# Kernel optimization log

Measured on AMD Instinct MI355X. Metric: run time of the kernel, lower is better.

Reference implementation:

```python
import jax, jax.numpy as jnp
from jax import lax
import numpy as np

B, S, D, H = 256, 4096, 64, 128  # batch, seq_len, input_dim, hidden_dim


def setup_inputs() -> dict:
    key = jax.random.key(0)
    ks = jax.random.split(key, 6)
    s_i = 1.0 / np.sqrt(D)
    s_h = 1.0 / np.sqrt(H)
    return {
        "x": jax.random.normal(ks[0], (B, S, D), dtype=jnp.float32),
        "Wi": jax.random.uniform(ks[1], (D, 4 * H), jnp.float32, -s_i, s_i),  # input->gates, no bias (flax LSTMCell)
        "Wh": jax.random.uniform(ks[2], (H, 4 * H), jnp.float32, -s_h, s_h),  # hidden->gates
        "bh": jnp.zeros((4 * H,), jnp.float32),
        "Wo": jax.random.uniform(ks[3], (H, 1), jnp.float32, -s_h, s_h),      # output Dense
        "bo": jnp.zeros((1,), jnp.float32),
    }


def reference(x, Wi, Wh, bh, Wo, bo):
    b, s, _ = x.shape
    h_dim = Wh.shape[0]
    # Precompute the input-path gate projections for all timesteps at once.
    xg = jnp.einsum('bsd,dg->sbg', x, Wi)  # [S, B, 4H]

    def step(carry, xg_t):
        c, h = carry
        z = xg_t + h @ Wh + bh  # [B, 4H]
        i, f, g, o = jnp.split(z, 4, axis=-1)
        i = jax.nn.sigmoid(i)
        f = jax.nn.sigmoid(f)
        g = jnp.tanh(g)
        o = jax.nn.sigmoid(o)
        c_new = f * c + i * g
        h_new = o * jnp.tanh(c_new)
        return (c_new, h_new), None

    c0 = jnp.zeros((b, h_dim), x.dtype)
    h0 = jnp.zeros((b, h_dim), x.dtype)
    (c_last, h_last), _ = lax.scan(step, (c0, h0), xg)
    # project last hidden state -> (batch, 1)
    return h_last @ Wo + bo
```

## Files before the change

### kernel.cpp

```cpp
#include <hip/hip_runtime.h>
#include <hip/hip_fp16.h>


#define LSTM_B 256
#define LSTM_S 4096
#define LSTM_D 64
#define LSTM_H 128
#define LSTM_G 512

typedef _Float16 f16x8 __attribute__((ext_vector_type(8)));
typedef float f32x4 __attribute__((ext_vector_type(4)));

__device__ __forceinline__ float sigm(float z) {
  return __builtin_amdgcn_rcpf(1.0f + __builtin_amdgcn_exp2f(-1.44269504f * z));
}
__device__ __forceinline__ float tanh_(float z) {
  return 1.0f - 2.0f * __builtin_amdgcn_rcpf(1.0f + __builtin_amdgcn_exp2f(2.88539008f * z));
}

__global__ __launch_bounds__(256, 1)
void lstm_mfma_kernel(const float* __restrict__ x,
                      const float* __restrict__ Wi,
                      const float* __restrict__ Wh,
                      const float* __restrict__ bh,
                      const float* __restrict__ Wo,
                      const float* __restrict__ bo,
                      float* __restrict__ out) {
  const int t    = threadIdx.x;
  const int lane = t & 63;
  const int w    = t >> 6;
  const int b    = blockIdx.x;
  const int lmod = lane & 15;
  const int lgrp = lane >> 4;

  __shared__ __align__(16) _Float16 Hbuf[2][LSTM_H];
  __shared__ __align__(16) _Float16 Xbuf[2][LSTM_D];
  __shared__ __align__(16) _Float16 Zr[8];
  __shared__ float R[LSTM_H];

  f16x8 Bf[8][6];
  #pragma unroll
  for (int g = 0; g < 4; ++g) {
    #pragma unroll
    for (int hh = 0; hh < 2; ++hh) {
      const int nt = 2 * g + hh;
      const int n = 128 * g + 32 * w + 16 * hh + lmod;
      #pragma unroll
      for (int kk = 0; kk < 6; ++kk) {
        union { f16x8 v; _Float16 e[8]; } uB;
        #pragma unroll
        for (int j = 0; j < 8; ++j) {
          const int k = 32 * kk + 8 * lgrp + j;
          const float val = (k < LSTM_H) ? Wh[(size_t)k * LSTM_G + n]
                                         : Wi[(size_t)(k - LSTM_H) * LSTM_G + n];
          uB.e[j] = (_Float16)val;
        }
        Bf[nt][kk] = uB.v;
      }
    }
  }

  const int ul = 32 * w + (lane & 31);
  const float bb0 = bh[ul];
  const float bb1 = bh[LSTM_H + ul];
  const float bb2 = bh[2 * LSTM_H + ul];
  const float bb3 = bh[3 * LSTM_H + ul];

  const float* xb = x + (size_t)b * (LSTM_S * LSTM_D);
  const bool areal = (lmod == 0) || (lmod == 4);

  const f32x4 ZQ = {0.f, 0.f, 0.f, 0.f};

  if (t < LSTM_H) Hbuf[0][t] = (_Float16)0.0f;
  if (w == 1) Xbuf[0][lane] = (_Float16)xb[lane];
  if (w == 2) Xbuf[1][lane] = (_Float16)xb[LSTM_D + lane];
  if (t < 8) Zr[t] = (_Float16)0.0f;
  __syncthreads();

  f16x8 X0a, X0b, X1a, X1b;
  f32x4 accP[8], accQ[8];
  {
    const char* a0 = areal ? ((const char*)&Xbuf[0][0] + 16 * lgrp)
                           : (const char*)&Zr[0];
    const int s0 = areal ? 64 : 0;
    f16x8 T0 = *(const f16x8*)(a0);
    f16x8 T1 = *(const f16x8*)(a0 + s0);
    const char* a1 = areal ? ((const char*)&Xbuf[1][0] + 16 * lgrp)
                           : (const char*)&Zr[0];
    X0a = *(const f16x8*)(a1);
    X0b = *(const f16x8*)(a1 + s0);
    #pragma unroll
    for (int n = 0; n < 8; ++n) {
      accP[n] = __builtin_amdgcn_mfma_f32_16x16x32_f16(T0, Bf[n][4], ZQ, 0, 0, 0);
      accP[n] = __builtin_amdgcn_mfma_f32_16x16x32_f16(T1, Bf[n][5], accP[n], 0, 0, 0);
    }
  }
  __syncthreads();
  if (w == 1) Xbuf[0][lane] = (_Float16)xb[2 * LSTM_D + lane];
  float xA = 0.f, xB = 0.f;
  if (w == 3) {
    xA = xb[3 * LSTM_D + lane];
    xB = xb[4 * LSTM_D + lane];
  }
  float c = 0.f, hval = 0.f;
  __syncthreads();

  #define STEPB(P, ACCIN, ACCOUT, XC0, XC1, XN0, XN1)                          \
  {                                                                            \
    float xn = 0.f;                                                            \
    if (w == 3) {                                                              \
      int si = s + 5; if (si > LSTM_S - 1) si = LSTM_S - 1;                    \
      xn = xb[(size_t)si * LSTM_D + lane];                                     \
    }                                                                          \
    const char* ahB = areal ? ((const char*)&Hbuf[P][0] + 16 * lgrp)           \
                            : (const char*)&Zr[0];                             \
    const int ahS = areal ? 64 : 0;                                            \
    f16x8 Ah0 = *(const f16x8*)(ahB);                                          \
    f16x8 Ah1 = *(const f16x8*)(ahB + 1 * ahS);                                \
    f16x8 Ah2 = *(const f16x8*)(ahB + 2 * ahS);                                \
    f16x8 Ah3 = *(const f16x8*)(ahB + 3 * ahS);                                \
    const char* axB = areal ? ((const char*)&Xbuf[P][0] + 16 * lgrp)           \
                            : (const char*)&Zr[0];                             \
    XN0 = *(const f16x8*)(axB);                                                \
    XN1 = *(const f16x8*)(axB + ahS);                                          \
    __builtin_amdgcn_sched_barrier(0);                                         \
    _Pragma("unroll")                                                          \
    for (int n = 0; n < 8; ++n)                                                \
      ACCOUT[n] = __builtin_amdgcn_mfma_f32_16x16x32_f16(XC0, Bf[n][4], ZQ, 0, 0, 0); \
    _Pragma("unroll")                                                          \
    for (int n = 0; n < 8; ++n)                                                \
      ACCOUT[n] = __builtin_amdgcn_mfma_f32_16x16x32_f16(XC1, Bf[n][5], ACCOUT[n], 0, 0, 0); \
    __builtin_amdgcn_sched_barrier(0);                                         \
    _Pragma("unroll")                                                          \
    for (int n = 0; n < 8; ++n)                                                \
      ACCIN[n] = __builtin_amdgcn_mfma_f32_16x16x32_f16(Ah0, Bf[n][0], ACCIN[n], 0, 0, 0); \
    _Pragma("unroll")                                                          \
    for (int n = 0; n < 8; ++n)                                                \
      ACCIN[n] = __builtin_amdgcn_mfma_f32_16x16x32_f16(Ah1, Bf[n][1], ACCIN[n], 0, 0, 0); \
    _Pragma("unroll")                                                          \
    for (int n = 0; n < 8; ++n)                                                \
      ACCIN[n] = __builtin_amdgcn_mfma_f32_16x16x32_f16(Ah2, Bf[n][2], ACCIN[n], 0, 0, 0); \
    _Pragma("unroll")                                                          \
    for (int n = 0; n < 8; ++n)                                                \
      ACCIN[n] = __builtin_amdgcn_mfma_f32_16x16x32_f16(Ah3, Bf[n][3], ACCIN[n], 0, 0, 0); \
    {                                                                          \
      const bool hsel = (lane & 16) != 0;                                      \
      const float zi = (hsel ? ACCIN[1][0] : ACCIN[0][0]) + bb0;               \
      const float zf = (hsel ? ACCIN[3][0] : ACCIN[2][0]) + bb1;               \
      const float zg = (hsel ? ACCIN[5][0] : ACCIN[4][0]) + bb2;               \
      const float zo = (hsel ? ACCIN[7][0] : ACCIN[6][0]) + bb3;               \
      const float iv = sigm(zi);                                               \
      const float fv = sigm(zf);                                               \
      const float gv = tanh_(zg);                                              \
      const float ov = sigm(zo);                                               \
      c = fv * c + iv * gv;                                                    \
      hval = ov * tanh_(c);                                                    \
      if (lane < 32) Hbuf[(P) ^ 1][ul] = (_Float16)hval;                       \
    }                                                                          \
    if (w == 3) {                                                              \
      Xbuf[(P) ^ 1][lane] = (_Float16)xA;                                      \
      xA = xB;                                                                 \
      xB = xn;                                                                 \
    }                                                                          \
    __syncthreads();                                                           \
  }

  for (int s = 0; s < LSTM_S; s += 2) {
    STEPB(0, accP, accQ, X0a, X0b, X1a, X1b)
    ++s;
    STEPB(1, accQ, accP, X1a, X1b, X0a, X0b)
    --s;
  }
  #undef STEPB

  if (lane < 32) R[ul] = hval * Wo[ul];
  __syncthreads();
  if (t < 64) {
    float v = R[t] + R[t + 64];
    #pragma unroll
    for (int off = 32; off; off >>= 1) v += __shfl_down(v, off);
    if (t == 0) out[b] = v + bo[0];
  }
}

extern "C" void kernel_launch(void* const* d_in, const int* in_sizes, int n_in,
                              void* d_out, int out_size, void* d_ws, size_t ws_size,
                              hipStream_t stream) {
  const float* x  = (const float*)d_in[0];
  const float* Wi = (const float*)d_in[1];
  const float* Wh = (const float*)d_in[2];
  const float* bh = (const float*)d_in[3];
  const float* Wo = (const float*)d_in[4];
  const float* bo = (const float*)d_in[5];
  float* out = (float*)d_out;

  lstm_mfma_kernel<<<LSTM_B, 256, 0, stream>>>(x, Wi, Wh, bh, Wo, bo, out);
}
```

Baseline: 2.216 ms.

## Split LSTM gate columns across eight waves instead of four per block

Each block now runs 512 threads (8 waves). Each wave owns 16 hidden units and computes 4 MFMA N-tiles per step instead of 8, which halves the per-wave serial MFMA chain on the recurrent critical path. The cost is more waves synchronising at every timestep barrier. The 8 waves also share the SIMDs, so MFMA throughput per CU may not improve, and only 16 lanes per wave now do the gate math.

```diff
diff --git a/kernel.cpp b/kernel.cpp
--- a/kernel.cpp
+++ b/kernel.cpp
@@ -11,6 +11,8 @@
 typedef _Float16 f16x8 __attribute__((ext_vector_type(8)));
 typedef float f32x4 __attribute__((ext_vector_type(4)));
 
+#define SBAR() __builtin_amdgcn_sched_barrier(0)
+
 __device__ __forceinline__ float sigm(float z) {
   return __builtin_amdgcn_rcpf(1.0f + __builtin_amdgcn_exp2f(-1.44269504f * z));
 }
@@ -18,7 +20,7 @@
   return 1.0f - 2.0f * __builtin_amdgcn_rcpf(1.0f + __builtin_amdgcn_exp2f(2.88539008f * z));
 }
 
-__global__ __launch_bounds__(256, 1)
+__global__ __launch_bounds__(512, 2)
 void lstm_mfma_kernel(const float* __restrict__ x,
                       const float* __restrict__ Wi,
                       const float* __restrict__ Wh,
@@ -38,36 +40,32 @@
   __shared__ __align__(16) _Float16 Zr[8];
   __shared__ float R[LSTM_H];
 
-  f16x8 Bf[8][6];
+  f16x8 Bf[4][6];
   #pragma unroll
   for (int g = 0; g < 4; ++g) {
+    const int n = 128 * g + 16 * w + lmod;
     #pragma unroll
-    for (int hh = 0; hh < 2; ++hh) {
-      const int nt = 2 * g + hh;
-      const int n = 128 * g + 32 * w + 16 * hh + lmod;
+    for (int kk = 0; kk < 6; ++kk) {
+      union { f16x8 v; _Float16 e[8]; } uB;
       #pragma unroll
-      for (int kk = 0; kk < 6; ++kk) {
-        union { f16x8 v; _Float16 e[8]; } uB;
-        #pragma unroll
-        for (int j = 0; j < 8; ++j) {
-          const int k = 32 * kk + 8 * lgrp + j;
-          const float val = (k < LSTM_H) ? Wh[(size_t)k * LSTM_G + n]
-                                         : Wi[(size_t)(k - LSTM_H) * LSTM_G + n];
-          uB.e[j] = (_Float16)val;
-        }
-        Bf[nt][kk] = uB.v;
+      for (int j = 0; j < 8; ++j) {
+        const int k = 32 * kk + 8 * lgrp + j;
+        const float val = (k < LSTM_H) ? Wh[(size_t)k * LSTM_G + n]
+                                       : Wi[(size_t)(k - LSTM_H) * LSTM_G + n];
+        uB.e[j] = (_Float16)val;
       }
+      Bf[g][kk] = uB.v;
     }
   }
 
-  const int ul = 32 * w + (lane & 31);
+  const int ul = 16 * w + lmod;
   const float bb0 = bh[ul];
   const float bb1 = bh[LSTM_H + ul];
   const float bb2 = bh[2 * LSTM_H + ul];
   const float bb3 = bh[3 * LSTM_H + ul];
 
   const float* xb = x + (size_t)b * (LSTM_S * LSTM_D);
-  const bool areal = (lmod == 0) || (lmod == 4);
+  const bool areal = (lmod == 0);
 
   const f32x4 ZQ = {0.f, 0.f, 0.f, 0.f};
 
@@ -78,7 +76,7 @@
   __syncthreads();
 
   f16x8 X0a, X0b, X1a, X1b;
-  f32x4 accP[8], accQ[8];
+  f32x4 accP[4], accQ[4];
   {
     const char* a0 = areal ? ((const char*)&Xbuf[0][0] + 16 * lgrp)
                            : (const char*)&Zr[0];
@@ -90,25 +88,27 @@
     X0a = *(const f16x8*)(a1);
     X0b = *(const f16x8*)(a1 + s0);
     #pragma unroll
-    for (int n = 0; n < 8; ++n) {
-      accP[n] = __builtin_amdgcn_mfma_f32_16x16x32_f16(T0, Bf[n][4], ZQ, 0, 0, 0);
-      accP[n] = __builtin_amdgcn_mfma_f32_16x16x32_f16(T1, Bf[n][5], accP[n], 0, 0, 0);
+    for (int g = 0; g < 4; ++g) {
+      accP[g] = __builtin_amdgcn_mfma_f32_16x16x32_f16(T0, Bf[g][4], ZQ, 0, 0, 0);
+      accP[g] = __builtin_amdgcn_mfma_f32_16x16x32_f16(T1, Bf[g][5], accP[g], 0, 0, 0);
     }
   }
   __syncthreads();
   if (w == 1) Xbuf[0][lane] = (_Float16)xb[2 * LSTM_D + lane];
   float xA = 0.f, xB = 0.f;
-  if (w == 3) {
+  if (w == 7) {
     xA = xb[3 * LSTM_D + lane];
     xB = xb[4 * LSTM_D + lane];
   }
   float c = 0.f, hval = 0.f;
   __syncthreads();
 
+  #define MFM(A_, B_, C_) __builtin_amdgcn_mfma_f32_16x16x32_f16(A_, B_, C_, 0, 0, 0)
+
   #define STEPB(P, ACCIN, ACCOUT, XC0, XC1, XN0, XN1)                          \
   {                                                                            \
     float xn = 0.f;                                                            \
-    if (w == 3) {                                                              \
+    if (w == 7) {                                                              \
       int si = s + 5; if (si > LSTM_S - 1) si = LSTM_S - 1;                    \
       xn = xb[(size_t)si * LSTM_D + lane];                                     \
     }                                                                          \
@@ -123,41 +123,40 @@
                             : (const char*)&Zr[0];                             \
     XN0 = *(const f16x8*)(axB);                                                \
     XN1 = *(const f16x8*)(axB + ahS);                                          \
-    __builtin_amdgcn_sched_barrier(0);                                         \
+    SBAR();                                                                    \
     _Pragma("unroll")                                                          \
-    for (int n = 0; n < 8; ++n)                                                \
-      ACCOUT[n] = __builtin_amdgcn_mfma_f32_16x16x32_f16(XC0, Bf[n][4], ZQ, 0, 0, 0); \
+    for (int g = 0; g < 4; ++g)                                                \
+      ACCOUT[g] = MFM(XC0, Bf[g][4], ZQ);                                      \
     _Pragma("unroll")                                                          \
-    for (int n = 0; n < 8; ++n)                                                \
-      ACCOUT[n] = __builtin_amdgcn_mfma_f32_16x16x32_f16(XC1, Bf[n][5], ACCOUT[n], 0, 0, 0); \
-    __builtin_amdgcn_sched_barrier(0);                                         \
+    for (int g = 0; g < 4; ++g)                                                \
+      ACCOUT[g] = MFM(XC1, Bf[g][5], ACCOUT[g]);                               \
+    SBAR();                                                                    \
     _Pragma("unroll")                                                          \
-    for (int n = 0; n < 8; ++n)                                                \
-      ACCIN[n] = __builtin_amdgcn_mfma_f32_16x16x32_f16(Ah0, Bf[n][0], ACCIN[n], 0, 0, 0); \
+    for (int g = 0; g < 4; ++g)                                                \
+      ACCIN[g] = MFM(Ah0, Bf[g][0], ACCIN[g]);                                 \
     _Pragma("unroll")                                                          \
-    for (int n = 0; n < 8; ++n)                                                \
-      ACCIN[n] = __builtin_amdgcn_mfma_f32_16x16x32_f16(Ah1, Bf[n][1], ACCIN[n], 0, 0, 0); \
+    for (int g = 0; g < 4; ++g)                                                \
+      ACCIN[g] = MFM(Ah1, Bf[g][1], ACCIN[g]);                                 \
     _Pragma("unroll")                                                          \
-    for (int n = 0; n < 8; ++n)                                                \
-      ACCIN[n] = __builtin_amdgcn_mfma_f32_16x16x32_f16(Ah2, Bf[n][2], ACCIN[n], 0, 0, 0); \
+    for (int g = 0; g < 4; ++g)                                                \
+      ACCIN[g] = MFM(Ah2, Bf[g][2], ACCIN[g]);                                 \
     _Pragma("unroll")                                                          \
-    for (int n = 0; n < 8; ++n)                                                \
-      ACCIN[n] = __builtin_amdgcn_mfma_f32_16x16x32_f16(Ah3, Bf[n][3], ACCIN[n], 0, 0, 0); \
+    for (int g = 0; g < 4; ++g)                                                \
+      ACCIN[g] = MFM(Ah3, Bf[g][3], ACCIN[g]);                                 \
     {                                                                          \
-      const bool hsel = (lane & 16) != 0;                                      \
-      const float zi = (hsel ? ACCIN[1][0] : ACCIN[0][0]) + bb0;               \
-      const float zf = (hsel ? ACCIN[3][0] : ACCIN[2][0]) + bb1;               \
-      const float zg = (hsel ? ACCIN[5][0] : ACCIN[4][0]) + bb2;               \
-      const float zo = (hsel ? ACCIN[7][0] : ACCIN[6][0]) + bb3;               \
+      const float zi = ACCIN[0][0] + bb0;                                      \
+      const float zf = ACCIN[1][0] + bb1;                                      \
+      const float zg = ACCIN[2][0] + bb2;                                      \
+      const float zo = ACCIN[3][0] + bb3;                                      \
       const float iv = sigm(zi);                                               \
       const float fv = sigm(zf);                                               \
       const float gv = tanh_(zg);                                              \
       const float ov = sigm(zo);                                               \
       c = fv * c + iv * gv;                                                    \
       hval = ov * tanh_(c);                                                    \
-      if (lane < 32) Hbuf[(P) ^ 1][ul] = (_Float16)hval;                       \
+      if (lane < 16) Hbuf[(P) ^ 1][ul] = (_Float16)hval;                       \
     }                                                                          \
-    if (w == 3) {                                                              \
+    if (w == 7) {                                                              \
       Xbuf[(P) ^ 1][lane] = (_Float16)xA;                                      \
       xA = xB;                                                                 \
       xB = xn;                                                                 \
@@ -172,8 +171,9 @@
     --s;
   }
   #undef STEPB
+  #undef MFM
 
-  if (lane < 32) R[ul] = hval * Wo[ul];
+  if (lane < 16) R[ul] = hval * Wo[ul];
   __syncthreads();
   if (t < 64) {
     float v = R[t] + R[t + 64];
@@ -194,5 +194,5 @@
   const float* bo = (const float*)d_in[5];
   float* out = (float*)d_out;
 
-  lstm_mfma_kernel<<<LSTM_B, 256, 0, stream>>>(x, Wi, Wh, bh, Wo, bo, out);
+  lstm_mfma_kernel<<<LSTM_B, 512, 0, stream>>>(x, Wi, Wh, bh, Wo, bo, out);
 }
```

After: 2.280 ms. 1.03x slower.
